# Kernel optimization log

Measured on AMD Instinct MI355X. Metric: run time of the kernel, lower is better.

## Reference

```python
import jax, jax.numpy as jnp
import numpy as np

NUM_HEADS = 16
HEAD_DIM = 128
ROT_DIM = 128  # rotary_emb_dim == head_dim
ROPE_BASE = 10000.0


def setup_inputs() -> dict:
    key = jax.random.key(0)
    k1, k2, k3, k4, k5 = jax.random.split(key, 5)
    b, s, d = 2, 2048, 2048
    return {
        "x": jax.random.normal(k1, (b, s, d), jnp.float32),
        "Wqkv_w": jax.random.normal(k2, (3 * d, d), jnp.float32) * (d ** -0.5),
        "Wqkv_b": jax.random.normal(k3, (3 * d,), jnp.float32) * 0.02,
        "wo_w": jax.random.normal(k4, (d, d), jnp.float32) * (d ** -0.5),
        "wo_b": jax.random.normal(k5, (d,), jnp.float32) * 0.02,
    }


def _deinterleave(t):
    # torch.cat([t[..., ::2], t[..., 1::2]], dim=-1)
    return jnp.concatenate([t[..., ::2], t[..., 1::2]], axis=-1)


def _rope(t, cos, sin):
    # non-interleaved (GPT-NeoX style) rotary on first ROT_DIM dims; here ROT_DIM == head_dim
    half = ROT_DIM // 2
    x1, x2 = t[..., :half], t[..., half:ROT_DIM]
    # cos/sin: (s, half) -> broadcast over (b, s, h, half)
    c = cos[None, :, None, :]
    sn = sin[None, :, None, :]
    return jnp.concatenate([x1 * c - x2 * sn, x2 * c + x1 * sn], axis=-1)


def reference(x, Wqkv_w, Wqkv_b, wo_w, wo_b):
    b, s, d = x.shape
    h, hd = NUM_HEADS, HEAD_DIM
    # fused QKV projection, layout '(h three d)' per original rearrange
    qkv = x @ Wqkv_w.T + Wqkv_b                      # (b, s, 3*d)
    qkv = qkv.reshape(b, s, h, 3, hd)
    q = _deinterleave(qkv[:, :, :, 0, :])            # (b, s, h, hd)
    k = _deinterleave(qkv[:, :, :, 1, :])
    v = qkv[:, :, :, 2, :]
    # rotary embedding tables
    inv_freq = 1.0 / (ROPE_BASE ** (jnp.arange(0, ROT_DIM, 2, dtype=jnp.float32) / ROT_DIM))
    freqs = jnp.arange(s, dtype=jnp.float32)[:, None] * inv_freq[None, :]  # (s, half)
    cos, sin = jnp.cos(freqs), jnp.sin(freqs)
    q = _rope(q, cos, sin)
    k = _rope(k, cos, sin)
    # causal self-attention (SelfAttention, softmax_scale = 1/sqrt(hd))
    scale = hd ** -0.5
    scores = jnp.einsum('bshd,bthd->bhst', q, k) * scale  # (b, h, s, s)
    mask = jnp.tril(jnp.ones((s, s), dtype=bool))
    scores = jnp.where(mask[None, None], scores, jnp.finfo(scores.dtype).min)
    probs = jax.nn.softmax(scores, axis=-1)
    ctx = jnp.einsum('bhst,bthd->bshd', probs, v)    # (b, s, h, hd)
    ctx = ctx.reshape(b, s, d)
    return ctx @ wo_w.T + wo_b
```

## Files before the change

kernel.cpp:

```cpp
#include <hip/hip_runtime.h>

#define B_ 2
#define S_ 2048
#define H_ 16
#define HD_ 128
#define QKVROW 6144
#define M_ 4096

typedef float f32x4 __attribute__((ext_vector_type(4)));
typedef __bf16 bf16x8 __attribute__((ext_vector_type(8)));
typedef unsigned short ushortx8 __attribute__((ext_vector_type(8)));

__device__ __forceinline__ float bf2f(unsigned short u) {
  union { unsigned u; float f; } v;
  v.u = ((unsigned)u) << 16;
  return v.f;
}
__device__ __forceinline__ unsigned short f2bf(float f) {
  union { __bf16 b; unsigned short u; } c;
  c.b = (__bf16)f;
  return c.u;
}
__device__ __forceinline__ ushortx8 cvt8(const float* f) {
  const f32x4 lo = *(const f32x4*)f;
  const f32x4 hi = *(const f32x4*)(f + 4);
  ushortx8 o;
#pragma unroll
  for (int t = 0; t < 4; ++t) o[t] = f2bf(lo[t]);
#pragma unroll
  for (int t = 0; t < 4; ++t) o[4 + t] = f2bf(hi[t]);
  return o;
}
__device__ __forceinline__ void async16(const unsigned short* g, unsigned short* l) {
  __builtin_amdgcn_global_load_lds(
      (const __attribute__((address_space(1))) unsigned int*)g,
      (__attribute__((address_space(3))) unsigned int*)l, 16, 0, 0);
}

__global__ __launch_bounds__(256) void rope_table(float* __restrict__ tab) {
  const int i = blockIdx.x * 256 + threadIdx.x;
  const int s = i >> 6, t = i & 63;
  const float invf = expf(-(float)t * 0.14391156831212787f);
  float sn, cs;
  sincosf((float)s * invf, &sn, &cs);
  tab[2 * i] = cs;
  tab[2 * i + 1] = sn;
}

__global__ __launch_bounds__(256) void f2bf3(
    const float* __restrict__ a, unsigned short* __restrict__ da, int na8,
    const float* __restrict__ b, unsigned short* __restrict__ db, int nb8,
    const float* __restrict__ c, unsigned short* __restrict__ dc, int nc8) {
  const int ntot = na8 + nb8 + nc8;
  int i = blockIdx.x * 256 + threadIdx.x;
  const int stride = gridDim.x * 256;
  for (; i < ntot; i += stride) {
    const float* s;
    unsigned short* d;
    int off = i;
    if (off < na8) { s = a; d = da; }
    else if (off - na8 < nb8) { off -= na8; s = b; d = db; }
    else { off -= na8 + nb8; s = c; d = dc; }
    const ushortx8 o = cvt8(s + (size_t)off * 8);
    *(ushortx8*)&d[(size_t)off * 8] = o;
  }
}

__global__ __launch_bounds__(256) void gemm1(
    const unsigned short* __restrict__ A, const unsigned short* __restrict__ Bm,
    const float* __restrict__ bias, unsigned short* __restrict__ C) {
  __shared__ unsigned short As[128 * 64];
  __shared__ unsigned short Bs[128 * 64];
  const int tid = threadIdx.x;
  const int lane = tid & 63, wave = tid >> 6;
  const int l15 = lane & 15, quad = lane >> 4;
  const int m0 = blockIdx.y * 128, n0 = blockIdx.x * 128;
  const int wr = (wave >> 1) * 64, wc = (wave & 1) * 64;

  f32x4 acc[4][4];
#pragma unroll
  for (int r = 0; r < 4; ++r)
#pragma unroll
    for (int c = 0; c < 4; ++c) acc[r][c] = (f32x4){0.f, 0.f, 0.f, 0.f};

  for (int k0 = 0; k0 < 2048; k0 += 64) {
    __syncthreads();
#pragma unroll
    for (int i = 0; i < 4; ++i) {
      const int c0 = wave * 256 + i * 64;
      const int u = c0 + lane;
      const int row = u >> 3, cu = u & 7;
      const int cs = cu ^ (row & 7);
      async16(A + (size_t)(m0 + row) * 2048 + k0 + cs * 8, &As[c0 * 8]);
      async16(Bm + (size_t)(n0 + row) * 2048 + k0 + cs * 8, &Bs[c0 * 8]);
    }
    __syncthreads();

#pragma unroll
    for (int s = 0; s < 2; ++s) {
      bf16x8 af[4], bf[4];
#pragma unroll
      for (int r = 0; r < 4; ++r) {
        const int row = wr + r * 16 + l15;
        af[r] = *(const bf16x8*)&As[row * 64 + (((s * 4 + quad) ^ (row & 7)) << 3)];
      }
#pragma unroll
      for (int c = 0; c < 4; ++c) {
        const int row = wc + c * 16 + l15;
        bf[c] = *(const bf16x8*)&Bs[row * 64 + (((s * 4 + quad) ^ (row & 7)) << 3)];
      }
#pragma unroll
      for (int r = 0; r < 4; ++r)
#pragma unroll
        for (int c = 0; c < 4; ++c)
          acc[r][c] = __builtin_amdgcn_mfma_f32_16x16x32_bf16(af[r], bf[c], acc[r][c], 0, 0, 0);
    }
  }

#pragma unroll
  for (int c = 0; c < 4; ++c) {
    const int col = n0 + wc + c * 16 + l15;
    const float bv = bias[col];
#pragma unroll
    for (int r = 0; r < 4; ++r) {
      const int row = m0 + wr + r * 16 + quad * 4;
#pragma unroll
      for (int i = 0; i < 4; ++i)
        C[(size_t)(row + i) * QKVROW + col] = f2bf(acc[r][c][i] + bv);
    }
  }
}

__global__ __launch_bounds__(256) void rope_vt(
    unsigned short* qkv, unsigned short* __restrict__ Vt,
    const float* __restrict__ tab) {
  __shared__ unsigned short vs[64 * 136];
  const int b = blockIdx.z, h = blockIdx.y, s0 = blockIdx.x * 64;
  const int tid = threadIdx.x;
  const int r = tid >> 2, cpart = (tid & 3) * 32;
  const int s = s0 + r;
  unsigned short* base = qkv + (size_t)(b * S_ + s) * QKVROW + h * 384;
  const int j0 = cpart >> 1;

  ushortx8 ivq[4], ivk[4], ivv[4];
#pragma unroll
  for (int i = 0; i < 4; ++i) {
    ivq[i] = *(const ushortx8*)&base[cpart + i * 8];
    ivk[i] = *(const ushortx8*)&base[128 + cpart + i * 8];
    ivv[i] = *(const ushortx8*)&base[256 + cpart + i * 8];
  }

  float cs[16], sn[16];
  {
    const f32x4* tr = (const f32x4*)&tab[(size_t)s * 128 + j0 * 2];
#pragma unroll
    for (int t = 0; t < 8; ++t) {
      const f32x4 v = tr[t];
      cs[2 * t] = v[0]; sn[2 * t] = v[1];
      cs[2 * t + 1] = v[2]; sn[2 * t + 1] = v[3];
    }
  }

  __syncthreads();

#pragma unroll
  for (int which = 0; which < 2; ++which) {
    const ushortx8* iv = (which == 0) ? ivq : ivk;
    const float scale = (which == 0) ? 0.08838834764831845f : 1.0f;
    ushortx8 o1a, o1b, o2a, o2b;
#pragma unroll
    for (int t = 0; t < 16; ++t) {
      const float x1 = bf2f(iv[(2 * t) >> 3][(2 * t) & 7]);
      const float x2 = bf2f(iv[(2 * t + 1) >> 3][(2 * t + 1) & 7]);
      const unsigned short r1 = f2bf((x1 * cs[t] - x2 * sn[t]) * scale);
      const unsigned short r2 = f2bf((x2 * cs[t] + x1 * sn[t]) * scale);
      if (t < 8) { o1a[t] = r1; o2a[t] = r2; }
      else       { o1b[t - 8] = r1; o2b[t - 8] = r2; }
    }
    unsigned short* out = base + which * 128;
    *(ushortx8*)&out[j0] = o1a;
    *(ushortx8*)&out[j0 + 8] = o1b;
    *(ushortx8*)&out[64 + j0] = o2a;
    *(ushortx8*)&out[64 + j0 + 8] = o2b;
  }

#pragma unroll
  for (int i = 0; i < 4; ++i)
    *(ushortx8*)&vs[r * 136 + cpart + i * 8] = ivv[i];
  __syncthreads();
  const size_t vtb = (size_t)(b * H_ + h) * HD_ * S_ + s0;
#pragma unroll
  for (int it = 0; it < 4; ++it) {
    const int a = tid + it * 256;
    const int d = a >> 3, sc = (a & 7) * 8;
    ushortx8 o;
#pragma unroll
    for (int t = 0; t < 8; ++t) o[t] = vs[(sc + t) * 136 + d];
    *(ushortx8*)&Vt[vtb + (size_t)d * S_ + sc] = o;
  }
}

__global__ __launch_bounds__(256) void attn(
    unsigned short* qkv, const unsigned short* __restrict__ Vt) {
  __shared__ unsigned short Ks[64 * 136];
  __shared__ unsigned short Vs[128 * 72];
  __shared__ unsigned short Ps[4 * 16 * 72];
  const int p = blockIdx.x, sub = blockIdx.y, bh = blockIdx.z;
  const int b = bh >> 4, h = bh & 15;
  const int tid = threadIdx.x, lane = tid & 63, wave = tid >> 6;
  const int l15 = lane & 15, quad = lane >> 4;

  unsigned short* qh = qkv + (size_t)b * S_ * QKVROW + h * 384;
  const unsigned short* Vb = Vt + (size_t)bh * HD_ * S_;
  unsigned short* Pw = &Ps[wave * 16 * 72];

  ushortx8 rk[4], rv[4];
  auto pref = [&](int j) {
#pragma unroll
    for (int t = 0; t < 4; ++t) {
      const int uk = t * 256 + tid;
      const int krow = uk >> 4, kcu = uk & 15;
      rk[t] = *(const ushortx8*)(qh + (size_t)(j * 64 + krow) * QKVROW + 128 + kcu * 8);
      const int vrow = uk >> 3, vcu = uk & 7;
      rv[t] = *(const ushortx8*)(Vb + (size_t)vrow * S_ + j * 64 + vcu * 8);
    }
  };
  pref(0);

#pragma unroll
  for (int half = 0; half < 2; ++half) {
    const int qt = half ? 15 - p : p;
    const int jN = 2 * qt + 1 + sub;
    const int r0 = qt * 128 + sub * 64 + wave * 16;

    bf16x8 aq[4];
#pragma unroll
    for (int ks = 0; ks < 4; ++ks)
      aq[ks] = *(const bf16x8*)&qh[(size_t)(r0 + l15) * QKVROW + ks * 32 + quad * 8];

    f32x4 o[8];
    float mrow[4], lrow[4];
#pragma unroll
    for (int ct = 0; ct < 8; ++ct) o[ct] = (f32x4){0.f, 0.f, 0.f, 0.f};
#pragma unroll
    for (int i = 0; i < 4; ++i) { mrow[i] = -1e30f; lrow[i] = 0.f; }

    for (int j = 0; j < jN; ++j) {
      __syncthreads();
#pragma unroll
      for (int t = 0; t < 4; ++t) {
        const int uk = t * 256 + tid;
        *(ushortx8*)&Ks[(uk >> 4) * 136 + (uk & 15) * 8] = rk[t];
        *(ushortx8*)&Vs[(uk >> 3) * 72 + (uk & 7) * 8] = rv[t];
      }
      __syncthreads();

      const int jn = (j + 1 < jN) ? j + 1 : (half == 0 ? 0 : -1);
      if (jn >= 0) pref(jn);

      f32x4 sacc[4];
#pragma unroll
      for (int ct = 0; ct < 4; ++ct) sacc[ct] = (f32x4){0.f, 0.f, 0.f, 0.f};
#pragma unroll
      for (int ks = 0; ks < 4; ++ks) {
        bf16x8 bk[4];
#pragma unroll
        for (int ct = 0; ct < 4; ++ct)
          bk[ct] = *(const bf16x8*)&Ks[(ct * 16 + l15) * 136 + ks * 32 + quad * 8];
#pragma unroll
        for (int ct = 0; ct < 4; ++ct)
          sacc[ct] = __builtin_amdgcn_mfma_f32_16x16x32_bf16(aq[ks], bk[ct], sacc[ct], 0, 0, 0);
      }

      if (j >= 2 * qt) {
#pragma unroll
        for (int ct = 0; ct < 4; ++ct)
#pragma unroll
          for (int i = 0; i < 4; ++i) {
            const int grow = r0 + quad * 4 + i;
            const int gcol = j * 64 + ct * 16 + l15;
            if (gcol > grow) sacc[ct][i] = -1e30f;
          }
      }

#pragma unroll
      for (int i = 0; i < 4; ++i) {
        float m = sacc[0][i];
#pragma unroll
        for (int ct = 1; ct < 4; ++ct) m = fmaxf(m, sacc[ct][i]);
#pragma unroll
        for (int off = 1; off < 16; off <<= 1) m = fmaxf(m, __shfl_xor(m, off));
        const float mn = fmaxf(mrow[i], m);
        const float alpha = __expf(mrow[i] - mn);
        mrow[i] = mn;
        float rsum = 0.f;
#pragma unroll
        for (int ct = 0; ct < 4; ++ct) {
          const float pv = __expf(sacc[ct][i] - mn);
          sacc[ct][i] = pv;
          rsum += pv;
        }
#pragma unroll
        for (int off = 1; off < 16; off <<= 1) rsum += __shfl_xor(rsum, off);
        lrow[i] = lrow[i] * alpha + rsum;
#pragma unroll
        for (int ct = 0; ct < 8; ++ct) o[ct][i] *= alpha;
      }

#pragma unroll
      for (int ct = 0; ct < 4; ++ct)
#pragma unroll
        for (int i = 0; i < 4; ++i)
          Pw[(quad * 4 + i) * 72 + ct * 16 + l15] = f2bf(sacc[ct][i]);

#pragma unroll
      for (int ks = 0; ks < 2; ++ks) {
        const bf16x8 ap = *(const bf16x8*)&Pw[l15 * 72 + ks * 32 + quad * 8];
        bf16x8 bv[8];
#pragma unroll
        for (int ct = 0; ct < 8; ++ct)
          bv[ct] = *(const bf16x8*)&Vs[(ct * 16 + l15) * 72 + ks * 32 + quad * 8];
#pragma unroll
        for (int ct = 0; ct < 8; ++ct)
          o[ct] = __builtin_amdgcn_mfma_f32_16x16x32_bf16(ap, bv[ct], o[ct], 0, 0, 0);
      }
    }

    float inv[4];
#pragma unroll
    for (int i = 0; i < 4; ++i) inv[i] = 1.0f / lrow[i];
#pragma unroll
    for (int ct = 0; ct < 8; ++ct)
#pragma unroll
      for (int i = 0; i < 4; ++i) {
        const int srow = r0 + quad * 4 + i;
        qh[(size_t)srow * QKVROW + ct * 16 + l15] = f2bf(o[ct][i] * inv[i]);
      }
  }
}

__global__ __launch_bounds__(256) void gemm2(
    const unsigned short* __restrict__ A, const unsigned short* __restrict__ Bm,
    const float* __restrict__ bias, float* __restrict__ C) {
  __shared__ unsigned short As[128 * 64];
  __shared__ unsigned short Bs[128 * 64];
  const int tid = threadIdx.x;
  const int lane = tid & 63, wave = tid >> 6;
  const int l15 = lane & 15, quad = lane >> 4;
  const int m0 = blockIdx.y * 128, n0 = blockIdx.x * 128;
  const int wr = (wave >> 1) * 64, wc = (wave & 1) * 64;

  f32x4 acc[4][4];
#pragma unroll
  for (int r = 0; r < 4; ++r)
#pragma unroll
    for (int c = 0; c < 4; ++c) acc[r][c] = (f32x4){0.f, 0.f, 0.f, 0.f};

  for (int k0 = 0; k0 < 2048; k0 += 64) {
    const int kh = ((k0 >> 7) * 384) + (k0 & 127);
    __syncthreads();
#pragma unroll
    for (int i = 0; i < 4; ++i) {
      const int c0 = wave * 256 + i * 64;
      const int u = c0 + lane;
      const int row = u >> 3, cu = u & 7;
      const int cs = cu ^ (row & 7);
      async16(A + (size_t)(m0 + row) * QKVROW + kh + cs * 8, &As[c0 * 8]);
      async16(Bm + (size_t)(n0 + row) * 2048 + k0 + cs * 8, &Bs[c0 * 8]);
    }
    __syncthreads();

#pragma unroll
    for (int s = 0; s < 2; ++s) {
      bf16x8 af[4], bf[4];
#pragma unroll
      for (int r = 0; r < 4; ++r) {
        const int row = wr + r * 16 + l15;
        af[r] = *(const bf16x8*)&As[row * 64 + (((s * 4 + quad) ^ (row & 7)) << 3)];
      }
#pragma unroll
      for (int c = 0; c < 4; ++c) {
        const int row = wc + c * 16 + l15;
        bf[c] = *(const bf16x8*)&Bs[row * 64 + (((s * 4 + quad) ^ (row & 7)) << 3)];
      }
#pragma unroll
      for (int r = 0; r < 4; ++r)
#pragma unroll
        for (int c = 0; c < 4; ++c)
          acc[r][c] = __builtin_amdgcn_mfma_f32_16x16x32_bf16(af[r], bf[c], acc[r][c], 0, 0, 0);
    }
  }

#pragma unroll
  for (int c = 0; c < 4; ++c) {
    const int col = n0 + wc + c * 16 + l15;
    const float bv = bias[col];
#pragma unroll
    for (int r = 0; r < 4; ++r) {
      const int row = m0 + wr + r * 16 + quad * 4;
#pragma unroll
      for (int i = 0; i < 4; ++i)
        C[(size_t)(row + i) * 2048 + col] = acc[r][c][i] + bv;
    }
  }
}

extern "C" void kernel_launch(void* const* d_in, const int* in_sizes, int n_in,
                              void* d_out, int out_size, void* d_ws, size_t ws_size,
                              hipStream_t stream) {
  const float* x    = (const float*)d_in[0];
  const float* wqkv = (const float*)d_in[1];
  const float* bqkv = (const float*)d_in[2];
  const float* wo   = (const float*)d_in[3];
  const float* bo   = (const float*)d_in[4];
  float* out = (float*)d_out;

  unsigned short* qkv = (unsigned short*)d_ws;
  unsigned short* Vt  = qkv + (size_t)M_ * QKVROW;
  unsigned short* xb  = Vt  + (size_t)B_ * H_ * HD_ * S_;
  unsigned short* wb  = xb  + (size_t)M_ * 2048;
  unsigned short* wob = wb  + (size_t)QKVROW * 2048;
  float* tab = (float*)(wob + (size_t)2048 * 2048);

  rope_table<<<dim3((S_ * 64) / 256), 256, 0, stream>>>(tab);
  f2bf3<<<dim3(2048), 256, 0, stream>>>(x, xb, (M_ * 2048) / 8,
                                        wqkv, wb, (QKVROW * 2048) / 8,
                                        wo, wob, (2048 * 2048) / 8);

  gemm1<<<dim3(QKVROW / 128, M_ / 128), 256, 0, stream>>>(xb, wb, bqkv, qkv);
  rope_vt<<<dim3(S_ / 64, H_, B_), 256, 0, stream>>>(qkv, Vt, tab);
  attn<<<dim3(8, 2, B_ * H_), 256, 0, stream>>>(qkv, Vt);
  gemm2<<<dim3(2048 / 128, M_ / 128), 256, 0, stream>>>(qkv, wob, bo, out);
}
```

Baseline: 413.9 us.

## Lazy softmax rescaling, deferred row-sum reduction, MFMA priority and grid reorder

The attention kernel now rescales the output accumulator and running max only when some row's tile max exceeds the stored max by more than a threshold of 8, checked wave-wide. The per-tile cross-lane row-sum shuffle reduction is deferred to a single reduction at the end. s_setprio raises wave priority around the MFMA blocks, and the grid is reordered so that batch-head is the fastest-varying block index. Together these aim to cut the exp, multiply and shuffle work in the softmax inner loop and improve scheduling and L2 locality. In exchange, exp values can reach up to e^8 before rescaling, so bf16 P values and the fp32 accumulators carry a wider dynamic range.

```diff
diff --git a/kernel.cpp b/kernel.cpp
--- a/kernel.cpp
+++ b/kernel.cpp
@@ -205,7 +205,7 @@
   __shared__ unsigned short Ks[64 * 136];
   __shared__ unsigned short Vs[128 * 72];
   __shared__ unsigned short Ps[4 * 16 * 72];
-  const int p = blockIdx.x, sub = blockIdx.y, bh = blockIdx.z;
+  const int bh = blockIdx.x, p = blockIdx.y, sub = blockIdx.z;
   const int b = bh >> 4, h = bh & 15;
   const int tid = threadIdx.x, lane = tid & 63, wave = tid >> 6;
   const int l15 = lane & 15, quad = lane >> 4;
@@ -239,11 +239,11 @@
       aq[ks] = *(const bf16x8*)&qh[(size_t)(r0 + l15) * QKVROW + ks * 32 + quad * 8];
 
     f32x4 o[8];
-    float mrow[4], lrow[4];
+    float mrow[4], lpart[4];
 #pragma unroll
     for (int ct = 0; ct < 8; ++ct) o[ct] = (f32x4){0.f, 0.f, 0.f, 0.f};
 #pragma unroll
-    for (int i = 0; i < 4; ++i) { mrow[i] = -1e30f; lrow[i] = 0.f; }
+    for (int i = 0; i < 4; ++i) { mrow[i] = -1e30f; lpart[i] = 0.f; }
 
     for (int j = 0; j < jN; ++j) {
       __syncthreads();
@@ -261,6 +261,7 @@
       f32x4 sacc[4];
 #pragma unroll
       for (int ct = 0; ct < 4; ++ct) sacc[ct] = (f32x4){0.f, 0.f, 0.f, 0.f};
+      __builtin_amdgcn_s_setprio(1);
 #pragma unroll
       for (int ks = 0; ks < 4; ++ks) {
         bf16x8 bk[4];
@@ -271,6 +272,7 @@
         for (int ct = 0; ct < 4; ++ct)
           sacc[ct] = __builtin_amdgcn_mfma_f32_16x16x32_bf16(aq[ks], bk[ct], sacc[ct], 0, 0, 0);
       }
+      __builtin_amdgcn_s_setprio(0);
 
       if (j >= 2 * qt) {
 #pragma unroll
@@ -283,28 +285,38 @@
           }
       }
 
+      float tmax[4];
 #pragma unroll
       for (int i = 0; i < 4; ++i) {
-        float m = sacc[0][i];
-#pragma unroll
-        for (int ct = 1; ct < 4; ++ct) m = fmaxf(m, sacc[ct][i]);
+        float m = fmaxf(fmaxf(sacc[0][i], sacc[1][i]), fmaxf(sacc[2][i], sacc[3][i]));
 #pragma unroll
         for (int off = 1; off < 16; off <<= 1) m = fmaxf(m, __shfl_xor(m, off));
-        const float mn = fmaxf(mrow[i], m);
-        const float alpha = __expf(mrow[i] - mn);
-        mrow[i] = mn;
-        float rsum = 0.f;
+        tmax[i] = m;
+      }
+      bool need = false;
+#pragma unroll
+      for (int i = 0; i < 4; ++i) need = need || (tmax[i] > mrow[i] + 8.f);
+      if (__any(need)) {
+#pragma unroll
+        for (int i = 0; i < 4; ++i) {
+          const float mn = fmaxf(mrow[i], tmax[i]);
+          const float alpha = __expf(mrow[i] - mn);
+          mrow[i] = mn;
+          lpart[i] *= alpha;
+#pragma unroll
+          for (int ct = 0; ct < 8; ++ct) o[ct][i] *= alpha;
+        }
+      }
+#pragma unroll
+      for (int i = 0; i < 4; ++i) {
+        float rs = 0.f;
 #pragma unroll
         for (int ct = 0; ct < 4; ++ct) {
-          const float pv = __expf(sacc[ct][i] - mn);
+          const float pv = __expf(sacc[ct][i] - mrow[i]);
           sacc[ct][i] = pv;
-          rsum += pv;
+          rs += pv;
         }
-#pragma unroll
-        for (int off = 1; off < 16; off <<= 1) rsum += __shfl_xor(rsum, off);
-        lrow[i] = lrow[i] * alpha + rsum;
-#pragma unroll
-        for (int ct = 0; ct < 8; ++ct) o[ct][i] *= alpha;
+        lpart[i] += rs;
       }
 
 #pragma unroll
@@ -313,6 +325,7 @@
         for (int i = 0; i < 4; ++i)
           Pw[(quad * 4 + i) * 72 + ct * 16 + l15] = f2bf(sacc[ct][i]);
 
+      __builtin_amdgcn_s_setprio(1);
 #pragma unroll
       for (int ks = 0; ks < 2; ++ks) {
         const bf16x8 ap = *(const bf16x8*)&Pw[l15 * 72 + ks * 32 + quad * 8];
@@ -324,11 +337,17 @@
         for (int ct = 0; ct < 8; ++ct)
           o[ct] = __builtin_amdgcn_mfma_f32_16x16x32_bf16(ap, bv[ct], o[ct], 0, 0, 0);
       }
+      __builtin_amdgcn_s_setprio(0);
     }
 
     float inv[4];
 #pragma unroll
-    for (int i = 0; i < 4; ++i) inv[i] = 1.0f / lrow[i];
+    for (int i = 0; i < 4; ++i) {
+      float l = lpart[i];
+#pragma unroll
+      for (int off = 1; off < 16; off <<= 1) l += __shfl_xor(l, off);
+      inv[i] = 1.0f / l;
+    }
 #pragma unroll
     for (int ct = 0; ct < 8; ++ct)
 #pragma unroll
@@ -429,6 +448,6 @@
 
   gemm1<<<dim3(QKVROW / 128, M_ / 128), 256, 0, stream>>>(xb, wb, bqkv, qkv);
   rope_vt<<<dim3(S_ / 64, H_, B_), 256, 0, stream>>>(qkv, Vt, tab);
-  attn<<<dim3(8, 2, B_ * H_), 256, 0, stream>>>(qkv, Vt);
+  attn<<<dim3(B_ * H_, 8, 2), 256, 0, stream>>>(qkv, Vt);
   gemm2<<<dim3(2048 / 128, M_ / 128), 256, 0, stream>>>(qkv, wob, bo, out);
 }
```

Result: faster. 402.9 us, median of 2 (-2.7%).
